# Performance work log

Measured on AMD Instinct MI355X. Metric: run time of the kernel, lower is better.

Reference implementation:

```python
import jax, jax.numpy as jnp
import numpy as np

SQ = 1.0 / np.sqrt(2.0)

def _haar_filters():
    dec_lo = np.array([SQ, SQ], np.float32); dec_hi = np.array([-SQ, SQ], np.float32)
    rec_lo = np.array([SQ, SQ], np.float32); rec_hi = np.array([SQ, -SQ], np.float32)
    def bank(lo, hi):
        ks = []
        for fz in (lo, hi):
            for fy in (lo, hi):
                for fx in (lo, hi):
                    ks.append(np.einsum('i,j,k->ijk', fz, fy, fx))
        return jnp.asarray(np.stack(ks, 0))  # [8,2,2,2]
    return bank(dec_lo, dec_hi), bank(rec_lo, rec_hi)

WT_F, IWT_F = _haar_filters()

def dwt3(x):
    # stride-2 2x2x2 cross-correlation == reshape + einsum (kernel size == stride)
    B, C, D, H, W = x.shape
    xr = x.reshape(B, C, D // 2, 2, H // 2, 2, W // 2, 2)
    return jnp.einsum('bcdzhywx,fzyx->bcfdhw', xr, WT_F)  # [B,C,8,D/2,H/2,W/2]

def idwt3(x):
    # conv_transpose3d stride 2 kernel 2: no overlap -> einsum + reshape
    B, C, _, D, H, W = x.shape
    out = jnp.einsum('bcfdhw,fzyx->bcdzhywx', x, IWT_F)
    return out.reshape(B, C, 2 * D, 2 * H, 2 * W)

def dwconv3(x, w, b=None):
    # depthwise 3x3x3 conv, padding SAME (torch padding='same', groups=C)
    y = jax.lax.conv_general_dilated(
        x, w, (1, 1, 1), 'SAME',
        dimension_numbers=('NCDHW', 'OIDHW', 'NCDHW'),
        feature_group_count=x.shape[1])
    if b is not None:
        y = y + b[None, :, None, None, None]
    return y

WT_LEVELS = 2

def setup_inputs() -> dict:
    key = jax.random.key(0)
    ks = jax.random.split(key, 6)
    B, C, D, H, W = 1, 64, 64, 64, 64
    return {
        'x': jax.random.normal(ks[0], (B, C, D, H, W), jnp.float32),
        'base_w': jax.random.normal(ks[1], (C, 1, 3, 3, 3), jnp.float32) * 0.1,
        'base_b': jax.random.normal(ks[2], (C,), jnp.float32) * 0.02,
        'base_scale_w': jnp.ones((1, C, 1, 1, 1), jnp.float32),
        'wconv_w0': jax.random.normal(ks[3], (C * 8, 1, 3, 3, 3), jnp.float32) * 0.1,
        'wconv_w1': jax.random.normal(ks[4], (C * 8, 1, 3, 3, 3), jnp.float32) * 0.1,
        'wscale0': jnp.full((1, C * 8, 1, 1, 1), 0.1, jnp.float32),
        'wscale1': jnp.full((1, C * 8, 1, 1, 1), 0.1, jnp.float32),
        'lambd': jnp.float32(0.05),
    }

def reference(x, base_w, base_b, base_scale_w, wconv_w0, wconv_w1, wscale0, wscale1, lambd):
    wconv_ws = (wconv_w0, wconv_w1)
    wscales = (wscale0, wscale1)
    lls, hfs, shapes = [], [], []
    cur = x
    for i in range(WT_LEVELS):
        shapes.append(cur.shape)
        pd, ph, pw = cur.shape[2] % 2, cur.shape[3] % 2, cur.shape[4] % 2
        if pd or ph or pw:
            cur = jnp.pad(cur, ((0, 0), (0, 0), (0, pd), (0, ph), (0, pw)))
        cx = dwt3(cur)                     # [B,C,8,d,h,w]
        cur = cx[:, :, 0]                  # LL passes to next level
        B, C, _, d, h, w = cx.shape
        t = dwconv3(cx.reshape(B, C * 8, d, h, w), wconv_ws[i])
        t = t.reshape(B, C, 8, d, h, w)
        ll, hf = t[:, :, :1], t[:, :, 1:]
        hf = jnp.sign(hf) * jax.nn.relu(jnp.abs(hf) - lambd)  # soft threshold
        t = jnp.concatenate([ll, hf], axis=2)
        t = (t.reshape(B, C * 8, d, h, w) * wscales[i]).reshape(B, C, 8, d, h, w)
        lls.append(t[:, :, 0]); hfs.append(t[:, :, 1:])
    nxt = jnp.float32(0.0)
    for i in range(WT_LEVELS - 1, -1, -1):
        cll = lls[i] + nxt
        cx = jnp.concatenate([cll[:, :, None], hfs[i]], axis=2)
        nxt = idwt3(cx)
        sh = shapes[i]
        nxt = nxt[:, :, :sh[2], :sh[3], :sh[4]]
    base = dwconv3(x, base_w, base_b) * base_scale_w
    return base + nxt
```

## Files before the change

### kernel.cpp

```cpp
#include <hip/hip_runtime.h>

#define SQ3F 0.35355339059327379f

__device__ __forceinline__ float rfl(float v) {
    return __int_as_float(__builtin_amdgcn_readfirstlane(__float_as_int(v)));
}

__device__ __forceinline__ void haar_fwd(const float v[8], float o[8]) {
    float ax[8];
#pragma unroll
    for (int i = 0; i < 4; ++i) {
        float a = v[2 * i], b = v[2 * i + 1];
        ax[2 * i]     = a + b;
        ax[2 * i + 1] = b - a;
    }
    float ay[8];
#pragma unroll
    for (int z = 0; z < 2; ++z)
#pragma unroll
        for (int bx = 0; bx < 2; ++bx) {
            float a = ax[z * 4 + bx], b = ax[z * 4 + 2 + bx];
            ay[z * 4 + bx]     = a + b;
            ay[z * 4 + 2 + bx] = b - a;
        }
#pragma unroll
    for (int j = 0; j < 4; ++j) {
        float a = ay[j], b = ay[4 + j];
        o[j]     = (a + b) * SQ3F;
        o[4 + j] = (b - a) * SQ3F;
    }
}

__device__ __forceinline__ void haar_inv(const float t[8], float o[8]) {
    float az[8];
#pragma unroll
    for (int j = 0; j < 4; ++j) {
        float lo = t[j], hi = t[4 + j];
        az[j]     = lo + hi;
        az[4 + j] = lo - hi;
    }
    float ay[8];
#pragma unroll
    for (int z = 0; z < 2; ++z)
#pragma unroll
        for (int bx = 0; bx < 2; ++bx) {
            float lo = az[z * 4 + bx], hi = az[z * 4 + 2 + bx];
            ay[z * 4 + bx]     = lo + hi;
            ay[z * 4 + 2 + bx] = lo - hi;
        }
#pragma unroll
    for (int i = 0; i < 4; ++i) {
        float lo = ay[2 * i], hi = ay[2 * i + 1];
        o[2 * i]     = (lo + hi) * SQ3F;
        o[2 * i + 1] = (lo - hi) * SQ3F;
    }
}

__global__ __launch_bounds__(512, 6) void fused_l0_k(
    const float* __restrict__ x, const float* __restrict__ wt,
    const float* __restrict__ wscale, const float* __restrict__ lambd_p,
    float* __restrict__ t0, float* __restrict__ ll) {
    __shared__ __align__(16) float pl[8][32][36];
    int bx   = blockIdx.x;
    int slab = bx & 15;
    int c    = bx >> 4;
    int z0   = slab * 2;
    int tid  = threadIdx.x;

    {
        int fi   = tid >> 6;
        int rowi = (tid >> 1) & 31;
        pl[fi][rowi][(tid & 1) * 33] = 0.f;
    }

    int f    = __builtin_amdgcn_readfirstlane(tid >> 6);
    int lane = tid & 63;
    int cty  = lane >> 1;
    int cx0i = (lane & 1) * 16;
    int cc   = c * 8 + f;
    float wv[27];
    const float* wp = wt + cc * 27;
#pragma unroll
    for (int k = 0; k < 27; ++k) wv[k] = rfl(wp[k]);
    float lam = rfl(*lambd_p);
    float sc  = rfl(wscale[cc]);

    const float* xc = x + ((long)c << 18);

    float acc[2][16];
#pragma unroll
    for (int s = 0; s < 2; ++s)
#pragma unroll
        for (int j = 0; j < 16; ++j) acc[s][j] = 0.f;

#pragma unroll
    for (int pp = 0; pp < 4; ++pp) {
        int p       = z0 - 1 + pp;
        bool pvalid = (p >= 0) && (p <= 31);
        __syncthreads();
        if (pvalid) {
            int cell = 2 * tid;
            int y    = cell >> 5;
            int xx   = cell & 31;
            float v0[8], v1[8];
#pragma unroll
            for (int z = 0; z < 2; ++z)
#pragma unroll
                for (int yy = 0; yy < 2; ++yy) {
                    float4 q = *(const float4*)(xc + (((2 * p + z) << 6) +
                                                      (2 * y + yy)) * 64 + 2 * xx);
                    v0[z * 4 + yy * 2]     = q.x;
                    v0[z * 4 + yy * 2 + 1] = q.y;
                    v1[z * 4 + yy * 2]     = q.z;
                    v1[z * 4 + yy * 2 + 1] = q.w;
                }
            float o0[8], o1[8];
            haar_fwd(v0, o0);
            haar_fwd(v1, o1);
#pragma unroll
            for (int k = 0; k < 8; ++k) {
                pl[k][y][xx + 1] = o0[k];
                pl[k][y][xx + 2] = o1[k];
            }
            if (pp == 1 || pp == 2)
                *(float2*)(ll + (c << 15) + (p << 10) + cell) =
                    float2{o0[0], o1[0]};
        }
        __syncthreads();
        if (pvalid) {
#pragma unroll
            for (int dy = 0; dy < 3; ++dy) {
                int yy = cty - 1 + dy;
                if ((unsigned)yy < 32u) {
                    float r[18];
                    {
                        const float* rp = &pl[f][yy][cx0i];
                        float4 a0 = *(const float4*)(rp);
                        float4 a1 = *(const float4*)(rp + 4);
                        float4 a2 = *(const float4*)(rp + 8);
                        float4 a3 = *(const float4*)(rp + 12);
                        float2 a4 = *(const float2*)(rp + 16);
                        r[0]  = a0.x; r[1]  = a0.y; r[2]  = a0.z; r[3]  = a0.w;
                        r[4]  = a1.x; r[5]  = a1.y; r[6]  = a1.z; r[7]  = a1.w;
                        r[8]  = a2.x; r[9]  = a2.y; r[10] = a2.z; r[11] = a2.w;
                        r[12] = a3.x; r[13] = a3.y; r[14] = a3.z; r[15] = a3.w;
                        r[16] = a4.x; r[17] = a4.y;
                    }
#pragma unroll
                    for (int dz = 0; dz < 3; ++dz) {
                        int rel = pp - dz;
                        if (rel >= 0 && rel <= 1) {
#pragma unroll
                            for (int dx = 0; dx < 3; ++dx) {
                                float wgt = wv[dz * 9 + dy * 3 + dx];
#pragma unroll
                                for (int j = 0; j < 16; ++j)
                                    acc[rel][j] += r[dx + j] * wgt;
                            }
                        }
                    }
                }
            }
        }
        {
            int rel = pp - 2;
            if (rel >= 0 && rel <= 1) {
                int zc = z0 + rel;
                float res[16];
#pragma unroll
                for (int j = 0; j < 16; ++j) {
                    float t = acc[rel][j];
                    if (f != 0) {
                        float a = fabsf(t) - lam;
                        t       = a > 0.f ? copysignf(a, t) : 0.f;
                    }
                    res[j]      = t * sc;
                    acc[rel][j] = 0.f;
                }
                float* op = t0 + ((long)cc << 15) + (zc << 10) + cty * 32 + cx0i;
#pragma unroll
                for (int q = 0; q < 4; ++q)
                    *(float4*)(op + q * 4) = float4{res[q * 4], res[q * 4 + 1],
                                                    res[q * 4 + 2], res[q * 4 + 3]};
            }
        }
    }
}

template <int SO>
__global__ __launch_bounds__(256) void dwt3_k(const float* __restrict__ in,
                                              int inChStride,
                                              float* __restrict__ out) {
    constexpr int SI = SO * 2;
    int idx = blockIdx.x * 256 + threadIdx.x;
    int w = idx % SO;
    int h = (idx / SO) % SO;
    int d = (idx / (SO * SO)) % SO;
    int c = idx / (SO * SO * SO);
    const float* ip = in + (long)c * inChStride;
    float v[8];
#pragma unroll
    for (int z = 0; z < 2; ++z)
#pragma unroll
        for (int y = 0; y < 2; ++y) {
            const float2 p =
                *(const float2*)(ip + ((2 * d + z) * SI + (2 * h + y)) * SI + 2 * w);
            v[z * 4 + y * 2]     = p.x;
            v[z * 4 + y * 2 + 1] = p.y;
        }
    float o[8];
    haar_fwd(v, o);
    int s = (d * SO + h) * SO + w;
#pragma unroll
    for (int f = 0; f < 8; ++f) out[(c * 8 + f) * (SO * SO * SO) + s] = o[f];
}

template <int S, int PH>
__device__ __forceinline__ void conv_step(const float* __restrict__ ip, int zo,
                                          int ty, int x0,
                                          const float* __restrict__ wv,
                                          float win[3][3][6], float lam, float sc,
                                          bool hf, float* __restrict__ op) {
    constexpr int sPrev = (PH + 2) % 3;
    constexpr int sCur  = PH;
    constexpr int sNext = (PH + 1) % 3;
    {
        int zz = zo + 1;
        bool zok = zz < S;
        const float* pp = ip + zz * S * S;
#pragma unroll
        for (int dy = 0; dy < 3; ++dy) {
            int yy  = ty - 1 + dy;
            bool yok = zok && ((unsigned)yy < (unsigned)S);
            const float* rp = pp + yy * S;
            win[sNext][dy][0] = (yok && x0 > 0) ? rp[x0 - 1] : 0.f;
            float4 m = yok ? *(const float4*)(rp + x0) : float4{0.f, 0.f, 0.f, 0.f};
            win[sNext][dy][1] = m.x;
            win[sNext][dy][2] = m.y;
            win[sNext][dy][3] = m.z;
            win[sNext][dy][4] = m.w;
            win[sNext][dy][5] = (yok && (x0 + 4 < S)) ? rp[x0 + 4] : 0.f;
        }
    }
    float acc[4] = {0.f, 0.f, 0.f, 0.f};
#pragma unroll
    for (int dz = 0; dz < 3; ++dz) {
        const float(*wp)[6] = (dz == 0) ? win[sPrev] : (dz == 1) ? win[sCur] : win[sNext];
#pragma unroll
        for (int dy = 0; dy < 3; ++dy)
#pragma unroll
            for (int dx = 0; dx < 3; ++dx) {
                float wgt = wv[dz * 9 + dy * 3 + dx];
#pragma unroll
                for (int j = 0; j < 4; ++j) acc[j] += wp[dy][dx + j] * wgt;
            }
    }
    float4 r;
    float* rr = (float*)&r;
#pragma unroll
    for (int j = 0; j < 4; ++j) {
        float t = acc[j];
        if (hf) {
            float a = fabsf(t) - lam;
            t       = a > 0.f ? copysignf(a, t) : 0.f;
        }
        rr[j] = t * sc;
    }
    *(float4*)(op + (zo * S + ty) * S + x0) = r;
}

template <int S, int SLOT>
__device__ __forceinline__ void load_win_plane(const float* __restrict__ ip,
                                               int z, int ty, int x0,
                                               float win[3][3][6]) {
    bool zok = ((unsigned)z < (unsigned)S);
    const float* pp = ip + z * S * S;
#pragma unroll
    for (int dy = 0; dy < 3; ++dy) {
        int yy  = ty - 1 + dy;
        bool yok = zok && ((unsigned)yy < (unsigned)S);
        const float* rp = pp + yy * S;
        win[SLOT][dy][0] = (yok && x0 > 0) ? rp[x0 - 1] : 0.f;
        float4 m = yok ? *(const float4*)(rp + x0) : float4{0.f, 0.f, 0.f, 0.f};
        win[SLOT][dy][1] = m.x;
        win[SLOT][dy][2] = m.y;
        win[SLOT][dy][3] = m.z;
        win[SLOT][dy][4] = m.w;
        win[SLOT][dy][5] = (yok && (x0 + 4 < S)) ? rp[x0 + 4] : 0.f;
    }
}

template <int S, int PH0>
__device__ __forceinline__ void run_chunk(const float* __restrict__ ip, int z0,
                                          int ty, int x0,
                                          const float* __restrict__ wv,
                                          float win[3][3][6], float lam, float sc,
                                          bool hf, float* __restrict__ op) {
    load_win_plane<S, (PH0 + 2) % 3>(ip, z0 - 1, ty, x0, win);
    load_win_plane<S, PH0>(ip, z0, ty, x0, win);
    conv_step<S, PH0>(ip, z0, ty, x0, wv, win, lam, sc, hf, op);
    conv_step<S, (PH0 + 1) % 3>(ip, z0 + 1, ty, x0, wv, win, lam, sc, hf, op);
    conv_step<S, (PH0 + 2) % 3>(ip, z0 + 2, ty, x0, wv, win, lam, sc, hf, op);
    conv_step<S, PH0>(ip, z0 + 3, ty, x0, wv, win, lam, sc, hf, op);
}

template <int S, int CPB>
__global__ __launch_bounds__(256) void dwconv_soft_chunk_k(
    const float* __restrict__ in, const float* __restrict__ wt,
    const float* __restrict__ wscale, const float* __restrict__ lambd_p,
    float* __restrict__ out) {
    constexpr int TX = S / 4;
    int tid = threadIdx.x;
    int tx  = tid % TX;
    int ty  = (tid / TX) % S;
    int cs  = tid / (TX * S);
    int zc  = blockIdx.x & 3;
    int cg  = blockIdx.x >> 2;
    int cc  = cg * CPB + cs;
    const float* ip = in + (long)cc * (S * S * S);
    float* op       = out + (long)cc * (S * S * S);
    float wv[27];
#pragma unroll
    for (int k = 0; k < 27; ++k) wv[k] = wt[cc * 27 + k];
    float lam = *lambd_p;
    float sc  = wscale[cc];
    bool hf   = (cc & 7) != 0;
    int x0    = 4 * tx;

    float win[3][3][6];
    switch (zc) {
        case 0:  run_chunk<S, 0>(ip, 0,  ty, x0, wv, win, lam, sc, hf, op); break;
        case 1:  run_chunk<S, 1>(ip, 4,  ty, x0, wv, win, lam, sc, hf, op); break;
        case 2:  run_chunk<S, 2>(ip, 8,  ty, x0, wv, win, lam, sc, hf, op); break;
        default: run_chunk<S, 0>(ip, 12, ty, x0, wv, win, lam, sc, hf, op); break;
    }
}

__global__ __launch_bounds__(256, 3) void final_k2(
    const float* __restrict__ x, const float* __restrict__ t0,
    const float* __restrict__ t1, const float* __restrict__ bw,
    const float* __restrict__ bb, const float* __restrict__ bscale,
    float* __restrict__ out) {
    __shared__ float xs[18 * 10 * 67];
    int bx = blockIdx.x;
    int c  = bx >> 5;
    int ti = bx & 31;
    int dt = ti >> 3;
    int ht = ti & 7;
    const float* xc = x + ((long)c << 18);
    int zg0 = 16 * dt - 1, yg0 = 8 * ht - 1;
    for (int i = threadIdx.x; i < 18 * 10 * 66; i += 256) {
        int pz = i / 660;
        int r  = i - pz * 660;
        int py = r / 66;
        int px = r - py * 66;
        int zg = zg0 + pz, yg = yg0 + py, xg = px - 1;
        bool ok = ((unsigned)zg < 64u) && ((unsigned)yg < 64u) && ((unsigned)xg < 64u);
        xs[(pz * 10 + py) * 67 + px] = ok ? xc[(zg << 12) + (yg << 6) + xg] : 0.f;
    }
    const float* wp0 = bw + c * 27;
    float wv[27];
#pragma unroll
    for (int k = 0; k < 27; ++k) wv[k] = wp0[k];
    float bias = bb[c], scl = bscale[c];
    __syncthreads();

    int tid = threadIdx.x;
    int wc  = tid & 7;
    int hc  = (tid >> 3) & 3;
    int dc  = tid >> 5;
    int d   = dt * 8 + dc;
    int h   = ht * 4 + hc;
    int w0  = wc * 4;

    float acc[2][2][8];
#pragma unroll
    for (int oz = 0; oz < 2; ++oz)
#pragma unroll
        for (int oy = 0; oy < 2; ++oy)
#pragma unroll
            for (int m = 0; m < 8; ++m) acc[oz][oy][m] = 0.f;

#pragma unroll
    for (int pz = 0; pz < 4; ++pz) {
        float r[4][10];
#pragma unroll
        for (int py = 0; py < 4; ++py)
#pragma unroll
            for (int k = 0; k < 10; ++k)
                r[py][k] = xs[((2 * dc + pz) * 10 + (2 * hc + py)) * 67 + 8 * wc + k];
#pragma unroll
        for (int oz = 0; oz < 2; ++oz) {
            int kz = pz - oz;
            if (kz >= 0 && kz <= 2) {
#pragma unroll
                for (int py = 0; py < 4; ++py)
#pragma unroll
                    for (int oy = 0; oy < 2; ++oy) {
                        int ky = py - oy;
                        if (ky >= 0 && ky <= 2) {
#pragma unroll
                            for (int kx = 0; kx < 3; ++kx) {
                                float wgt = wv[kz * 9 + ky * 3 + kx];
#pragma unroll
                                for (int m = 0; m < 8; ++m)
                                    acc[oz][oy][m] += r[py][m + kx] * wgt;
                            }
                        }
                    }
            }
        }
    }

    int cell0 = (d << 10) + (h << 5) + w0;
    float4 t0v[8];
#pragma unroll
    for (int f = 0; f < 8; ++f)
        t0v[f] = *(const float4*)(t0 + (((long)(c * 8 + f)) << 15) + cell0);
    int s1b = ((d >> 1) * 16 + (h >> 1)) * 16 + (w0 >> 1);
    float2 t1v[8];
#pragma unroll
    for (int f = 0; f < 8; ++f)
        t1v[f] = *(const float2*)(t1 + ((c * 8 + f) << 12) + s1b);

#pragma unroll
    for (int j = 0; j < 4; ++j) {
        int w = w0 + j;
        float tf[8];
#pragma unroll
        for (int f = 0; f < 8; ++f) tf[f] = ((const float*)&t0v[f])[j];
        float add = 0.f;
#pragma unroll
        for (int f = 0; f < 8; ++f) {
            float v  = (j >> 1) ? t1v[f].y : t1v[f].x;
            float sg = 1.f;
            if ((f & 4) && (d & 1)) sg = -sg;
            if ((f & 2) && (h & 1)) sg = -sg;
            if ((f & 1) && (j & 1)) sg = -sg;
            add += sg * v;
        }
        tf[0] += add * SQ3F;
        float contrib[8];
        haar_inv(tf, contrib);
#pragma unroll
        for (int oz = 0; oz < 2; ++oz)
#pragma unroll
            for (int oy = 0; oy < 2; ++oy) {
                float2 rr;
                rr.x = (acc[oz][oy][2 * j] + bias) * scl + contrib[oz * 4 + oy * 2];
                rr.y = (acc[oz][oy][2 * j + 1] + bias) * scl +
                       contrib[oz * 4 + oy * 2 + 1];
                *(float2*)(out + ((long)c << 18) + ((2 * d + oz) << 12) +
                           ((2 * h + oy) << 6) + 2 * w) = rr;
            }
    }
}

extern "C" void kernel_launch(void* const* d_in, const int* in_sizes, int n_in,
                              void* d_out, int out_size, void* d_ws, size_t ws_size,
                              hipStream_t stream) {
    const float* x      = (const float*)d_in[0];
    const float* base_w = (const float*)d_in[1];
    const float* base_b = (const float*)d_in[2];
    const float* base_s = (const float*)d_in[3];
    const float* w0     = (const float*)d_in[4];
    const float* w1     = (const float*)d_in[5];
    const float* ws0    = (const float*)d_in[6];
    const float* ws1    = (const float*)d_in[7];
    const float* lambd  = (const float*)d_in[8];
    float* out = (float*)d_out;

    float* ll  = (float*)d_ws;
    float* t0  = ll + 2097152;
    float* cx1 = t0 + 16777216;
    float* t1  = cx1 + 2097152;

    fused_l0_k<<<1024, 512, 0, stream>>>(x, w0, ws0, lambd, t0, ll);
    dwt3_k<16><<<1024, 256, 0, stream>>>(ll, 32768, cx1);
    dwconv_soft_chunk_k<16, 4><<<512, 256, 0, stream>>>(cx1, w1, ws1, lambd, t1);
    final_k2<<<2048, 256, 0, stream>>>(x, t0, t1, base_w, base_b, base_s, out);
}
```

Baseline: 251.4 us.

## Fuse level-1 Haar DWT into level-0 kernel and remap block order

The second-level forward Haar transform now runs inside the level-0 fused kernel. The LL coefficients from the two planes are combined through cross-lane shuffles and written straight into cx1. This drops the separate dwt3 launch and the round trip of the LL intermediate through global memory. Block indices in the level-0 and level-1 conv kernels are also permuted, probably to spread channels across XCDs or caches. The cost is extra shuffles and scattered stores of cx1 in the fused kernel.

```diff
diff --git a/kernel.cpp b/kernel.cpp
--- a/kernel.cpp
+++ b/kernel.cpp
@@ -59,9 +59,9 @@
 __global__ __launch_bounds__(512, 6) void fused_l0_k(
     const float* __restrict__ x, const float* __restrict__ wt,
     const float* __restrict__ wscale, const float* __restrict__ lambd_p,
-    float* __restrict__ t0, float* __restrict__ ll) {
+    float* __restrict__ t0, float* __restrict__ cx1) {
     __shared__ __align__(16) float pl[8][32][36];
-    int bx   = blockIdx.x;
+    int bx   = ((blockIdx.x & 7) << 7) + (blockIdx.x >> 3);
     int slab = bx & 15;
     int c    = bx >> 4;
     int z0   = slab * 2;
@@ -92,6 +92,8 @@
     for (int s = 0; s < 2; ++s)
 #pragma unroll
         for (int j = 0; j < 16; ++j) acc[s][j] = 0.f;
+
+    float llq00 = 0.f, llq01 = 0.f;
 
 #pragma unroll
     for (int pp = 0; pp < 4; ++pp) {
@@ -122,9 +124,36 @@
                 pl[k][y][xx + 1] = o0[k];
                 pl[k][y][xx + 2] = o1[k];
             }
-            if (pp == 1 || pp == 2)
-                *(float2*)(ll + (c << 15) + (p << 10) + cell) =
-                    float2{o0[0], o1[0]};
+            if (pp == 1) {
+                llq00 = o0[0];
+                llq01 = o1[0];
+            }
+            if (pp == 2) {
+                float l10 = o0[0], l11 = o1[0];
+                float p00 = __shfl_xor(llq00, 16);
+                float p01 = __shfl_xor(llq01, 16);
+                float p10 = __shfl_xor(l10, 16);
+                float p11 = __shfl_xor(l11, 16);
+                int yp = (tid >> 4) & 1;
+                float v[8];
+                if (yp == 0) {
+                    v[0] = llq00; v[1] = llq01; v[2] = p00; v[3] = p01;
+                    v[4] = l10;   v[5] = l11;   v[6] = p10; v[7] = p11;
+                } else {
+                    v[0] = p00;   v[1] = p01;   v[2] = llq00; v[3] = llq01;
+                    v[4] = p10;   v[5] = p11;   v[6] = l10;   v[7] = l11;
+                }
+                float o[8];
+                haar_fwd(v, o);
+                int d  = z0 >> 1;
+                int hy = (tid >> 4) >> 1;
+                int wx = tid & 15;
+                int sA = (d * 16 + hy) * 16 + wx;
+                int f0 = yp * 4;
+#pragma unroll
+                for (int q = 0; q < 4; ++q)
+                    cx1[((c * 8 + f0 + q) << 12) + sA] = o[f0 + q];
+            }
         }
         __syncthreads();
         if (pvalid) {
@@ -187,34 +216,6 @@
     }
 }
 
-template <int SO>
-__global__ __launch_bounds__(256) void dwt3_k(const float* __restrict__ in,
-                                              int inChStride,
-                                              float* __restrict__ out) {
-    constexpr int SI = SO * 2;
-    int idx = blockIdx.x * 256 + threadIdx.x;
-    int w = idx % SO;
-    int h = (idx / SO) % SO;
-    int d = (idx / (SO * SO)) % SO;
-    int c = idx / (SO * SO * SO);
-    const float* ip = in + (long)c * inChStride;
-    float v[8];
-#pragma unroll
-    for (int z = 0; z < 2; ++z)
-#pragma unroll
-        for (int y = 0; y < 2; ++y) {
-            const float2 p =
-                *(const float2*)(ip + ((2 * d + z) * SI + (2 * h + y)) * SI + 2 * w);
-            v[z * 4 + y * 2]     = p.x;
-            v[z * 4 + y * 2 + 1] = p.y;
-        }
-    float o[8];
-    haar_fwd(v, o);
-    int s = (d * SO + h) * SO + w;
-#pragma unroll
-    for (int f = 0; f < 8; ++f) out[(c * 8 + f) * (SO * SO * SO) + s] = o[f];
-}
-
 template <int S, int PH>
 __device__ __forceinline__ void conv_step(const float* __restrict__ ip, int zo,
                                           int ty, int x0,
@@ -310,12 +311,13 @@
     const float* __restrict__ wscale, const float* __restrict__ lambd_p,
     float* __restrict__ out) {
     constexpr int TX = S / 4;
+    int bxl = ((blockIdx.x & 7) << 6) + (blockIdx.x >> 3);
     int tid = threadIdx.x;
     int tx  = tid % TX;
     int ty  = (tid / TX) % S;
     int cs  = tid / (TX * S);
-    int zc  = blockIdx.x & 3;
-    int cg  = blockIdx.x >> 2;
+    int zc  = bxl & 3;
+    int cg  = bxl >> 2;
     int cc  = cg * CPB + cs;
     const float* ip = in + (long)cc * (S * S * S);
     float* op       = out + (long)cc * (S * S * S);
@@ -470,13 +472,11 @@
     const float* lambd  = (const float*)d_in[8];
     float* out = (float*)d_out;
 
-    float* ll  = (float*)d_ws;
-    float* t0  = ll + 2097152;
+    float* t0  = (float*)d_ws;
     float* cx1 = t0 + 16777216;
     float* t1  = cx1 + 2097152;
 
-    fused_l0_k<<<1024, 512, 0, stream>>>(x, w0, ws0, lambd, t0, ll);
-    dwt3_k<16><<<1024, 256, 0, stream>>>(ll, 32768, cx1);
+    fused_l0_k<<<1024, 512, 0, stream>>>(x, w0, ws0, lambd, t0, cx1);
     dwconv_soft_chunk_k<16, 4><<<512, 256, 0, stream>>>(cx1, w1, ws1, lambd, t1);
     final_k2<<<2048, 256, 0, stream>>>(x, t0, t1, base_w, base_b, base_s, out);
 }
```

Result: no change. 249.6 us (-0.7%).
